# Performance work log

Measured on AMD Instinct MI355X. Metric: run time of the kernel, lower is better.

## Reference

```python
import jax, jax.numpy as jnp
import numpy as np

B, C, H, W = 4, 512, 64, 64
C8 = C // 8


def setup_inputs() -> dict:
    key = jax.random.key(0)
    ks = jax.random.split(key, 8)
    s = 0.02
    return {
        "x": jax.random.normal(ks[0], (B, C, H, W), dtype=jnp.float32),
        "wq": jax.random.normal(ks[1], (C8, C), dtype=jnp.float32) * s,
        "bq": jax.random.normal(ks[2], (C8,), dtype=jnp.float32) * s,
        "wk": jax.random.normal(ks[3], (C8, C), dtype=jnp.float32) * s,
        "bk": jax.random.normal(ks[4], (C8,), dtype=jnp.float32) * s,
        "wv": jax.random.normal(ks[5], (C, C), dtype=jnp.float32) * s,
        "bv": jax.random.normal(ks[6], (C,), dtype=jnp.float32) * s,
        "gamma": jax.random.normal(ks[7], (1,), dtype=jnp.float32),
    }


def reference(x, wq, bq, wk, bk, wv, bv, gamma):
    b, c, h, w = x.shape
    # 1x1 convs == per-pixel linear projections
    q = jnp.einsum('bchw,oc->bohw', x, wq) + bq[None, :, None, None]  # [B,C8,H,W]
    k = jnp.einsum('bchw,oc->bohw', x, wk) + bk[None, :, None, None]  # [B,C8,H,W]
    v = jnp.einsum('bchw,oc->bohw', x, wv) + bv[None, :, None, None]  # [B,C,H,W]
    qf = q.reshape(b, c // 8, h * w)  # [B,C8,HW]
    kf = k.reshape(b, c // 8, h * w)  # [B,C8,HW]
    # energy[b,i,j] = q_i . k_j, viewed as [B,H,W,H,W]; softmax over last dim
    energy = jnp.einsum('bci,bcj->bij', qf, kf).reshape(b, h, w, h, w)
    attn = jax.nn.softmax(energy, axis=-1)  # [B,H,W,H2,W2]
    # torch: out = bmm(value, permute(0,1,3,2,4).view(B,HW,HW))
    # rows index (h,h2) into value's spatial grid; cols index output (w,w2)
    out = jnp.einsum('bchk,bhwkv->bcwv', v, attn)  # [B,C,H,W]
    return gamma * out + x
```

## Files before the change

### kernel.cpp

```cpp
#include <hip/hip_runtime.h>
#include <hip/hip_bf16.h>


typedef __bf16 bf16_t;
typedef __bf16 bf16x8 __attribute__((ext_vector_type(8)));
typedef __bf16 bf16x4 __attribute__((ext_vector_type(4)));
typedef float f32x4 __attribute__((ext_vector_type(4)));

#define HW_ 4096
#define CIN 512
#define CQ 64

__device__ __forceinline__ void gload16(const void* g, void* l) {
  __builtin_amdgcn_global_load_lds((const __attribute__((address_space(1))) void*)g,
                                   (__attribute__((address_space(3))) void*)l, 16, 0, 0);
}

__global__ __launch_bounds__(256) void k_wcat(const float* __restrict__ wq,
                                              const float* __restrict__ wk,
                                              const float* __restrict__ wv,
                                              bf16_t* __restrict__ Wcat) {
  int idx = (blockIdx.x * 256 + threadIdx.x) * 4;
  int row = idx >> 9, c = idx & 511;
  const float* src;
  if (row < 64)       src = wq + row * 512 + c;
  else if (row < 128) src = wk + (row - 64) * 512 + c;
  else                src = wv + (row - 128) * 512 + c;
  float4 v = *(const float4*)src;
  bf16x4 o = { (bf16_t)v.x, (bf16_t)v.y, (bf16_t)v.z, (bf16_t)v.w };
  *(bf16x4*)&Wcat[idx] = o;
}

__global__ __launch_bounds__(256) void k_prep(const float* __restrict__ x, bf16_t* __restrict__ xT) {
  __shared__ float tile[64][65];
  const int b = blockIdx.z;
  const int p0 = blockIdx.x * 64, c0 = blockIdx.y * 64;
  const float* xb = x + (size_t)b * CIN * HW_;
  bf16_t* xTb = xT + (size_t)b * HW_ * CIN;
  const int tid = threadIdx.x;
  const int r = tid >> 4, q = tid & 15;
#pragma unroll
  for (int i = 0; i < 4; ++i) {
    int lr = r + 16 * i;
    float4 v = *(const float4*)&xb[(size_t)(c0 + lr) * HW_ + p0 + q * 4];
    tile[lr][q * 4 + 0] = v.x; tile[lr][q * 4 + 1] = v.y;
    tile[lr][q * 4 + 2] = v.z; tile[lr][q * 4 + 3] = v.w;
  }
  __syncthreads();
#pragma unroll
  for (int i = 0; i < 4; ++i) {
    int pr = r + 16 * i;
    bf16x4 o;
    o[0] = (bf16_t)tile[q * 4 + 0][pr];
    o[1] = (bf16_t)tile[q * 4 + 1][pr];
    o[2] = (bf16_t)tile[q * 4 + 2][pr];
    o[3] = (bf16_t)tile[q * 4 + 3][pr];
    *(bf16x4*)&xTb[(size_t)(p0 + pr) * CIN + c0 + q * 4] = o;
  }
}

__global__ __launch_bounds__(256) void k_proj(const bf16_t* __restrict__ Wcat,
                                              const bf16_t* __restrict__ xT,
                                              const float* __restrict__ bq,
                                              const float* __restrict__ bk,
                                              const float* __restrict__ bv,
                                              bf16_t* __restrict__ qfT2,
                                              bf16_t* __restrict__ kfT2,
                                              bf16_t* __restrict__ Vp2) {
  __shared__ bf16_t As[128][64];
  __shared__ bf16_t Bs[128][64];
  const int lin = blockIdx.x + blockIdx.y * 32 + blockIdx.z * 160;
  const int orig = (lin & 7) * 80 + (lin >> 3);
  const int by = orig % 5, bx = (orig / 5) & 31, b = orig / 160;
  const int n0 = bx * 128, m0 = by * 128;
  const char* Wb = (const char*)Wcat;
  const char* Xb = (const char*)(xT + (size_t)b * HW_ * CIN);
  const int tid = threadIdx.x, wv_ = tid >> 6, lane = tid & 63;
  const int wm = wv_ >> 1, wn = wv_ & 1;
  const int g = lane >> 4, cc = lane & 15;
  f32x4 acc[4][4]{};
  for (int ks = 0; ks < 512; ks += 64) {
    if (ks) __syncthreads();
#pragma unroll
    for (int i = 0; i < 4; ++i) {
      int ch = wv_ * 4 + i;
      int rr = ch * 8 + (lane >> 3);
      int sl = (lane & 7) ^ (rr & 7);
      int pix = (rr & 63) * 64 + (bx * 2) + (rr >> 6);
      gload16(Wb + (size_t)(m0 + rr) * 1024 + ks * 2 + sl * 16, (char*)As + ch * 1024);
      gload16(Xb + (size_t)pix * 1024 + ks * 2 + sl * 16, (char*)Bs + ch * 1024);
    }
    __syncthreads();
#pragma unroll
    for (int k2 = 0; k2 < 2; ++k2) {
      bf16x8 a[4], bb[4];
#pragma unroll
      for (int f = 0; f < 4; ++f)
        a[f] = *(const bf16x8*)((char*)As + (wm * 64 + f * 16 + cc) * 128 + (((k2 * 4 + g) ^ (cc & 7)) * 16));
#pragma unroll
      for (int f = 0; f < 4; ++f)
        bb[f] = *(const bf16x8*)((char*)Bs + (wn * 64 + f * 16 + cc) * 128 + (((k2 * 4 + g) ^ (cc & 7)) * 16));
#pragma unroll
      for (int fm = 0; fm < 4; ++fm)
#pragma unroll
        for (int fn = 0; fn < 4; ++fn)
          acc[fm][fn] = __builtin_amdgcn_mfma_f32_16x16x32_bf16(a[fm], bb[fn], acc[fm][fn], 0, 0, 0);
    }
  }
  bf16_t* qb = qfT2 + (size_t)b * HW_ * CQ;
  bf16_t* kb = kfT2 + (size_t)b * HW_ * CQ;
  bf16_t* Vb = Vp2 + (size_t)b * CIN * HW_;
#pragma unroll
  for (int fm = 0; fm < 4; ++fm) {
#pragma unroll
    for (int j = 0; j < 4; ++j) {
      int m = m0 + wm * 64 + fm * 16 + g * 4 + j;
      float bias = (m < 64) ? bq[m] : (m < 128) ? bk[m - 64] : bv[m - 128];
#pragma unroll
      for (int fn = 0; fn < 4; ++fn) {
        int n = n0 + wn * 64 + fn * 16 + cc;
        float val = acc[fm][fn][j] + bias;
        if (m < 64)       qb[(size_t)n * CQ + m] = (bf16_t)val;
        else if (m < 128) kb[(size_t)n * CQ + (m - 64)] = (bf16_t)val;
        else              Vb[(size_t)(m - 128) * HW_ + n] = (bf16_t)val;
      }
    }
  }
}

__global__ __launch_bounds__(256) void k_energy(const bf16_t* __restrict__ qfT2,
                                                const bf16_t* __restrict__ kfT2,
                                                bf16_t* __restrict__ Pt, int zbase) {
  __shared__ bf16_t Qs[8192];
  __shared__ bf16_t Ks[2][4096];
  const int lin = blockIdx.x + blockIdx.y * 32 + blockIdx.z * 512;
  const int total = 512 * gridDim.z, chunk = total >> 3;
  const int orig = (lin & 7) * chunk + (lin >> 3);
  const int bx = orig & 31, by = (orig >> 5) & 15, bz = orig >> 9;
  const int b = zbase + bz;
  const int w0 = bx * 2, ky0 = by * 4;
  const char* qb = (const char*)(qfT2 + (size_t)b * HW_ * CQ);
  const char* kb = (const char*)(kfT2 + (size_t)b * HW_ * CQ);
  bf16_t* Ptb = Pt + (size_t)bz * 16777216;
  const int tid = threadIdx.x, wv_ = tid >> 6, lane = tid & 63;
  const int g = lane >> 4, cc = lane & 15;

#pragma unroll
  for (int i = 0; i < 4; ++i) {
    int ch = wv_ * 4 + i;
    int rr = ch * 8 + (lane >> 3);
    int sl = (lane & 7) ^ (rr & 7);
    gload16(qb + (size_t)(w0 * 64 + rr) * 128 + sl * 16, (char*)Qs + ch * 1024);
  }
  const char* kSb[2];
#pragma unroll
  for (int i = 0; i < 2; ++i) {
    int ch = wv_ * 2 + i;
    int rr = ch * 8 + (lane >> 3);
    int sl = (lane & 7) ^ (rr & 7);
    kSb[i] = kb + (size_t)rr * 8192 + ky0 * 128 + sl * 16;
    gload16(kSb[i], (char*)Ks[0] + ch * 1024);
  }
  asm volatile("s_waitcnt vmcnt(0)" ::: "memory");
  __builtin_amdgcn_s_barrier();

  bf16x8 qf[2][2];
#pragma unroll
  for (int fm = 0; fm < 2; ++fm)
#pragma unroll
    for (int k2 = 0; k2 < 2; ++k2)
      qf[fm][k2] = *(const bf16x8*)((char*)Qs + (wv_ * 32 + fm * 16 + cc) * 128 +
                                    (((k2 * 4 + g) ^ (cc & 7)) * 16));

  const int w = w0 + (wv_ >> 1);
  for (int kq = 0; kq < 4; ++kq) {
    const int cur = kq & 1;
    if (kq < 3) {
      const int nxt = cur ^ 1;
#pragma unroll
      for (int i = 0; i < 2; ++i) {
        int ch = wv_ * 2 + i;
        gload16(kSb[i] + (kq + 1) * 128, (char*)Ks[nxt] + ch * 1024);
      }
      asm volatile("s_waitcnt vmcnt(2)" ::: "memory");
    } else {
      asm volatile("s_waitcnt vmcnt(0)" ::: "memory");
    }
    __builtin_amdgcn_s_barrier();

    f32x4 acc[2][4]{};
#pragma unroll
    for (int k2 = 0; k2 < 2; ++k2) {
      bf16x8 kf[4];
#pragma unroll
      for (int f = 0; f < 4; ++f)
        kf[f] = *(const bf16x8*)((char*)Ks[cur] + (f * 16 + cc) * 128 + (((k2 * 4 + g) ^ (cc & 7)) * 16));
#pragma unroll
      for (int fm = 0; fm < 2; ++fm)
#pragma unroll
        for (int fn = 0; fn < 4; ++fn)
          acc[fm][fn] = __builtin_amdgcn_mfma_f32_16x16x32_bf16(qf[fm][k2], kf[fn], acc[fm][fn], 0, 0, 0);
    }
#pragma unroll
    for (int fm = 0; fm < 2; ++fm) {
      float e[4][4], invj[4];
#pragma unroll
      for (int j = 0; j < 4; ++j) {
        float mx = fmaxf(fmaxf(acc[fm][0][j], acc[fm][1][j]), fmaxf(acc[fm][2][j], acc[fm][3][j]));
#pragma unroll
        for (int d = 1; d < 16; d <<= 1) mx = fmaxf(mx, __shfl_xor(mx, d, 64));
        float s = 0.f;
#pragma unroll
        for (int fn = 0; fn < 4; ++fn) { e[fn][j] = __expf(acc[fm][fn][j] - mx); s += e[fn][j]; }
#pragma unroll
        for (int d = 1; d < 16; d <<= 1) s += __shfl_xor(s, d, 64);
        invj[j] = __builtin_amdgcn_rcpf(s);
      }
      int h0 = (wv_ & 1) * 32 + fm * 16 + g * 4;
#pragma unroll
      for (int fn = 0; fn < 4; ++fn) {
        int v = fn * 16 + cc;
        bf16x4 pk = { (bf16_t)(e[fn][0] * invj[0]), (bf16_t)(e[fn][1] * invj[1]),
                      (bf16_t)(e[fn][2] * invj[2]), (bf16_t)(e[fn][3] * invj[3]) };
        *(bf16x4*)&Ptb[(((size_t)w * 64 + (ky0 + kq)) * 64 + v) * 64 + h0] = pk;
      }
    }
    asm volatile("s_waitcnt lgkmcnt(0)" ::: "memory");
    __builtin_amdgcn_s_barrier();
  }
}

#define KSTEP_S(s, cur, nxt) do {                                                            \
    _Pragma("unroll")                                                                        \
    for (int r = 0; r < 4; ++r)                                                              \
      gload16(aSb[r] + (size_t)((s) + 1) * 128, Ls + (nxt) * 49152 + (r * 8 + wv_) * 1024);  \
    _Pragma("unroll")                                                                        \
    for (int r = 0; r < 2; ++r)                                                              \
      gload16(bSb[r] + (size_t)((s) + 1) * 8192,                                             \
              Ls + (nxt) * 49152 + 32768 + (r * 8 + wv_) * 1024);                            \
    asm volatile("s_waitcnt vmcnt(6)" ::: "memory");                                         \
    __builtin_amdgcn_s_barrier();                                                            \
    COMPUTE(cur);                                                                            \
  } while (0)

#define COMPUTE(cur) do {                                                                    \
    const char* base_ = Ls + (cur) * 49152;                                                  \
    _Pragma("unroll")                                                                        \
    for (int k2 = 0; k2 < 2; ++k2) {                                                         \
      bf16x8 a[4], bb[4];                                                                    \
      _Pragma("unroll")                                                                      \
      for (int fm = 0; fm < 4; ++fm) a[fm] = *(const bf16x8*)(base_ + aoff[k2][fm]);         \
      _Pragma("unroll")                                                                      \
      for (int fn = 0; fn < 4; ++fn) bb[fn] = *(const bf16x8*)(base_ + boff[k2][fn]);        \
      _Pragma("unroll")                                                                      \
      for (int fm = 0; fm < 4; ++fm)                                                         \
        _Pragma("unroll")                                                                    \
        for (int fn = 0; fn < 4; ++fn)                                                       \
          acc[fm][fn] = __builtin_amdgcn_mfma_f32_16x16x32_bf16(a[fm], bb[fn], acc[fm][fn], 0, 0, 0); \
    }                                                                                        \
  } while (0)

__global__ __launch_bounds__(512) void k_out(const bf16_t* __restrict__ Vp2,
                                             const bf16_t* __restrict__ Pt,
                                             const float* __restrict__ x,
                                             const float* __restrict__ gamma,
                                             float* __restrict__ outp, int zbase) {
  __shared__ char Ls[147456];
  const int lin = blockIdx.x + (blockIdx.y << 1) + (blockIdx.z << 6);
  const int nwg8 = (gridDim.z == 4) ? 32 : 8;
  const int rsw = (lin & 7) * nwg8 + (lin >> 3);
  const int c0 = (rsw & 1) * 256;
  const int w0 = ((rsw >> 1) & 31) * 2;
  const int bz = (gridDim.z == 4) ? (rsw >> 6) : 0;
  const int b = zbase + bz;
  const char* Vb = (const char*)(Vp2 + (size_t)b * CIN * HW_);
  const char* Pb = (const char*)(Pt + (size_t)bz * 16777216);
  const int tid = threadIdx.x, wv_ = tid >> 6, lane = tid & 63;
  const int wm = wv_ >> 1, wn = wv_ & 1;
  const int g = lane >> 4, cc = lane & 15;

  const char* aSb[4]; const char* bSb[2];
#pragma unroll
  for (int r = 0; r < 4; ++r) {
    int L = (r * 8 + wv_) * 64 + lane;
    int arow = L >> 3, asl = (L & 7) ^ (arow & 7);
    aSb[r] = Vb + (size_t)(c0 + arow) * 8192 + asl * 16;
  }
#pragma unroll
  for (int r = 0; r < 2; ++r) {
    int L = (r * 8 + wv_) * 64 + lane;
    int ws = L >> 9, e = L & 511, v = e >> 3, bsl = (e & 7) ^ (v & 7);
    bSb[r] = Pb + (size_t)(w0 + ws) * 524288 + v * 128 + bsl * 16;
  }
  int aoff[2][4], boff[2][4];
#pragma unroll
  for (int k2 = 0; k2 < 2; ++k2) {
#pragma unroll
    for (int fm = 0; fm < 4; ++fm)
      aoff[k2][fm] = (wm * 64 + fm * 16 + cc) * 128 + (((k2 * 4 + g) ^ (cc & 7)) * 16);
#pragma unroll
    for (int fn = 0; fn < 4; ++fn)
      boff[k2][fn] = 32768 + wn * 8192 + (fn * 16 + cc) * 128 + (((k2 * 4 + g) ^ (cc & 7)) * 16);
  }

  f32x4 acc[4][4]{};
#pragma unroll
  for (int r = 0; r < 4; ++r) gload16(aSb[r], Ls + (r * 8 + wv_) * 1024);
#pragma unroll
  for (int r = 0; r < 2; ++r) gload16(bSb[r], Ls + 32768 + (r * 8 + wv_) * 1024);

  int s = 0;
#pragma unroll 1
  for (int t = 0; t < 21; ++t) {
    KSTEP_S(s, 0, 1);
    KSTEP_S(s + 1, 1, 2);
    KSTEP_S(s + 2, 2, 0);
    s += 3;
  }
  asm volatile("s_waitcnt vmcnt(0)" ::: "memory");
  __builtin_amdgcn_s_barrier();
  COMPUTE(0);

  const float gmm = gamma[0];
  const float* xb = x + (size_t)b * CIN * HW_;
  float* ob = outp + (size_t)b * CIN * HW_;
  const int w = w0 + wn;
#pragma unroll
  for (int fm = 0; fm < 4; ++fm) {
#pragma unroll
    for (int jj = 0; jj < 4; ++jj) {
      int c = c0 + wm * 64 + fm * 16 + g * 4 + jj;
#pragma unroll
      for (int fn = 0; fn < 4; ++fn) {
        int n = w * 64 + fn * 16 + cc;
        size_t idx = (size_t)c * HW_ + n;
        ob[idx] = gmm * acc[fm][fn][jj] + xb[idx];
      }
    }
  }
}

extern "C" void kernel_launch(void* const* d_in, const int* in_sizes, int n_in,
                              void* d_out, int out_size, void* d_ws, size_t ws_size,
                              hipStream_t stream) {
  const float* x  = (const float*)d_in[0];
  const float* wq = (const float*)d_in[1];
  const float* bq = (const float*)d_in[2];
  const float* wk = (const float*)d_in[3];
  const float* bk = (const float*)d_in[4];
  const float* wv = (const float*)d_in[5];
  const float* bv = (const float*)d_in[6];
  const float* gamma = (const float*)d_in[7];
  float* outp = (float*)d_out;
  char* ws = (char*)d_ws;
  size_t off = 0;
  bf16_t* xT   = (bf16_t*)(ws + off); off += (size_t)4 * HW_ * CIN * 2;
  bf16_t* Wcat = (bf16_t*)(ws + off); off += (size_t)640 * CIN * 2;
  bf16_t* qfT2 = (bf16_t*)(ws + off); off += (size_t)4 * HW_ * CQ * 2;
  bf16_t* kfT2 = (bf16_t*)(ws + off); off += (size_t)4 * HW_ * CQ * 2;
  bf16_t* Vp2  = (bf16_t*)(ws + off); off += (size_t)4 * CIN * HW_ * 2;
  bf16_t* Pt   = (bf16_t*)(ws + off);
  const size_t pbytes = (size_t)HW_ * HW_ * 2;
  const bool full = (ws_size >= off + 4 * pbytes);

  k_wcat<<<dim3(320), dim3(256), 0, stream>>>(wq, wk, wv, Wcat);
  k_prep<<<dim3(64, 8, 4), dim3(256), 0, stream>>>(x, xT);
  k_proj<<<dim3(32, 5, 4), dim3(256), 0, stream>>>(Wcat, xT, bq, bk, bv, qfT2, kfT2, Vp2);
  if (full) {
    k_energy<<<dim3(32, 16, 4), dim3(256), 0, stream>>>(qfT2, kfT2, Pt, 0);
    k_out<<<dim3(2, 32, 4), dim3(512), 0, stream>>>(Vp2, Pt, x, gamma, outp, 0);
  } else {
    for (int b = 0; b < 4; ++b) {
      k_energy<<<dim3(32, 16, 1), dim3(256), 0, stream>>>(qfT2, kfT2, Pt, b);
      k_out<<<dim3(2, 32, 1), dim3(512), 0, stream>>>(Vp2, Pt, x, gamma, outp, b);
    }
  }
}
```

Before: 157.7 us.

## Double-buffer projection GEMM loads and give energy blocks more key rows

```diff
diff --git a/kernel.cpp b/kernel.cpp
--- a/kernel.cpp
+++ b/kernel.cpp
@@ -67,8 +67,7 @@
                                               bf16_t* __restrict__ qfT2,
                                               bf16_t* __restrict__ kfT2,
                                               bf16_t* __restrict__ Vp2) {
-  __shared__ bf16_t As[128][64];
-  __shared__ bf16_t Bs[128][64];
+  __shared__ char Ls[65536];
   const int lin = blockIdx.x + blockIdx.y * 32 + blockIdx.z * 160;
   const int orig = (lin & 7) * 80 + (lin >> 3);
   const int by = orig % 5, bx = (orig / 5) & 31, b = orig / 160;
@@ -78,35 +77,65 @@
   const int tid = threadIdx.x, wv_ = tid >> 6, lane = tid & 63;
   const int wm = wv_ >> 1, wn = wv_ & 1;
   const int g = lane >> 4, cc = lane & 15;
+
+  const char* aSb[4]; const char* bSb[4];
+#pragma unroll
+  for (int r = 0; r < 4; ++r) {
+    int L = (r * 4 + wv_) * 64 + lane;
+    int rr = L >> 3, sl = (L & 7) ^ (rr & 7);
+    aSb[r] = Wb + (size_t)(m0 + rr) * 1024 + sl * 16;
+    int pix = (rr & 63) * 64 + bx * 2 + (rr >> 6);
+    bSb[r] = Xb + (size_t)pix * 1024 + sl * 16;
+  }
+  int aoff[2][4], boff[2][4];
+#pragma unroll
+  for (int k2 = 0; k2 < 2; ++k2) {
+#pragma unroll
+    for (int f = 0; f < 4; ++f) {
+      aoff[k2][f] = (wm * 64 + f * 16 + cc) * 128 + (((k2 * 4 + g) ^ (cc & 7)) * 16);
+      boff[k2][f] = 16384 + (wn * 64 + f * 16 + cc) * 128 + (((k2 * 4 + g) ^ (cc & 7)) * 16);
+    }
+  }
+
   f32x4 acc[4][4]{};
-  for (int ks = 0; ks < 512; ks += 64) {
-    if (ks) __syncthreads();
-#pragma unroll
-    for (int i = 0; i < 4; ++i) {
-      int ch = wv_ * 4 + i;
-      int rr = ch * 8 + (lane >> 3);
-      int sl = (lane & 7) ^ (rr & 7);
-      int pix = (rr & 63) * 64 + (bx * 2) + (rr >> 6);
-      gload16(Wb + (size_t)(m0 + rr) * 1024 + ks * 2 + sl * 16, (char*)As + ch * 1024);
-      gload16(Xb + (size_t)pix * 1024 + ks * 2 + sl * 16, (char*)Bs + ch * 1024);
-    }
-    __syncthreads();
+#pragma unroll
+  for (int r = 0; r < 4; ++r) gload16(aSb[r], Ls + (r * 4 + wv_) * 1024);
+#pragma unroll
+  for (int r = 0; r < 4; ++r) gload16(bSb[r], Ls + 16384 + (r * 4 + wv_) * 1024);
+
+  for (int s = 0; s < 8; ++s) {
+    const int cur = s & 1;
+    if (s < 7) {
+      const int nxt = cur ^ 1;
+#pragma unroll
+      for (int r = 0; r < 4; ++r)
+        gload16(aSb[r] + (size_t)(s + 1) * 128, Ls + nxt * 32768 + (r * 4 + wv_) * 1024);
+#pragma unroll
+      for (int r = 0; r < 4; ++r)
+        gload16(bSb[r] + (size_t)(s + 1) * 128, Ls + nxt * 32768 + 16384 + (r * 4 + wv_) * 1024);
+      asm volatile("s_waitcnt vmcnt(8)" ::: "memory");
+    } else {
+      asm volatile("s_waitcnt vmcnt(0)" ::: "memory");
+    }
+    __builtin_amdgcn_s_barrier();
+    const char* base = Ls + cur * 32768;
 #pragma unroll
     for (int k2 = 0; k2 < 2; ++k2) {
       bf16x8 a[4], bb[4];
 #pragma unroll
-      for (int f = 0; f < 4; ++f)
-        a[f] = *(const bf16x8*)((char*)As + (wm * 64 + f * 16 + cc) * 128 + (((k2 * 4 + g) ^ (cc & 7)) * 16));
-#pragma unroll
-      for (int f = 0; f < 4; ++f)
-        bb[f] = *(const bf16x8*)((char*)Bs + (wn * 64 + f * 16 + cc) * 128 + (((k2 * 4 + g) ^ (cc & 7)) * 16));
+      for (int f = 0; f < 4; ++f) a[f] = *(const bf16x8*)(base + aoff[k2][f]);
+#pragma unroll
+      for (int f = 0; f < 4; ++f) bb[f] = *(const bf16x8*)(base + boff[k2][f]);
 #pragma unroll
       for (int fm = 0; fm < 4; ++fm)
 #pragma unroll
         for (int fn = 0; fn < 4; ++fn)
           acc[fm][fn] = __builtin_amdgcn_mfma_f32_16x16x32_bf16(a[fm], bb[fn], acc[fm][fn], 0, 0, 0);
     }
-  }
+    asm volatile("s_waitcnt lgkmcnt(0)" ::: "memory");
+    __builtin_amdgcn_s_barrier();
+  }
+
   bf16_t* qb = qfT2 + (size_t)b * HW_ * CQ;
   bf16_t* kb = kfT2 + (size_t)b * HW_ * CQ;
   bf16_t* Vb = Vp2 + (size_t)b * CIN * HW_;
@@ -133,12 +162,12 @@
                                                 bf16_t* __restrict__ Pt, int zbase) {
   __shared__ bf16_t Qs[8192];
   __shared__ bf16_t Ks[2][4096];
-  const int lin = blockIdx.x + blockIdx.y * 32 + blockIdx.z * 512;
-  const int total = 512 * gridDim.z, chunk = total >> 3;
+  const int lin = blockIdx.x + blockIdx.y * 32 + blockIdx.z * 256;
+  const int total = 256 * gridDim.z, chunk = total >> 3;
   const int orig = (lin & 7) * chunk + (lin >> 3);
-  const int bx = orig & 31, by = (orig >> 5) & 15, bz = orig >> 9;
+  const int bx = orig & 31, by = (orig >> 5) & 7, bz = orig >> 8;
   const int b = zbase + bz;
-  const int w0 = bx * 2, ky0 = by * 4;
+  const int w0 = bx * 2, ky0 = by * 8;
   const char* qb = (const char*)(qfT2 + (size_t)b * HW_ * CQ);
   const char* kb = (const char*)(kfT2 + (size_t)b * HW_ * CQ);
   bf16_t* Ptb = Pt + (size_t)bz * 16777216;
@@ -173,9 +202,9 @@
                                     (((k2 * 4 + g) ^ (cc & 7)) * 16));
 
   const int w = w0 + (wv_ >> 1);
-  for (int kq = 0; kq < 4; ++kq) {
+  for (int kq = 0; kq < 8; ++kq) {
     const int cur = kq & 1;
-    if (kq < 3) {
+    if (kq < 7) {
       const int nxt = cur ^ 1;
 #pragma unroll
       for (int i = 0; i < 2; ++i) {
@@ -367,11 +396,11 @@
   k_prep<<<dim3(64, 8, 4), dim3(256), 0, stream>>>(x, xT);
   k_proj<<<dim3(32, 5, 4), dim3(256), 0, stream>>>(Wcat, xT, bq, bk, bv, qfT2, kfT2, Vp2);
   if (full) {
-    k_energy<<<dim3(32, 16, 4), dim3(256), 0, stream>>>(qfT2, kfT2, Pt, 0);
+    k_energy<<<dim3(32, 8, 4), dim3(256), 0, stream>>>(qfT2, kfT2, Pt, 0);
     k_out<<<dim3(2, 32, 4), dim3(512), 0, stream>>>(Vp2, Pt, x, gamma, outp, 0);
   } else {
     for (int b = 0; b < 4; ++b) {
-      k_energy<<<dim3(32, 16, 1), dim3(256), 0, stream>>>(qfT2, kfT2, Pt, b);
+      k_energy<<<dim3(32, 8, 1), dim3(256), 0, stream>>>(qfT2, kfT2, Pt, b);
       k_out<<<dim3(2, 32, 1), dim3(512), 0, stream>>>(Vp2, Pt, x, gamma, outp, b);
     }
   }
```

Measured after the change: 162.1 us. 2.8% more time.
